# Kernel tuning notes

Hardware: AMD Instinct MI355X
Metric: run time of the kernel (lower is better)

Reference implementation:

```python
import jax, jax.numpy as jnp
import numpy as np

FILTER_SIZE = 7
IMG = 256
MID = FILTER_SIZE // 2
# base coefficient per tap: -((r-m)^2 + (c-m)^2) / 2, flattened over the k*k window
_BASE = np.array([-(((r - MID) ** 2 + (c - MID) ** 2) / 2.0)
                  for r in range(FILTER_SIZE) for c in range(FILTER_SIZE)],
                 dtype=np.float32)


def setup_inputs() -> dict:
    key = jax.random.key(0)
    k1, k2 = jax.random.split(key)
    x = jax.random.normal(k1, (16, 3, IMG, IMG), dtype=jnp.float32)
    sigma = jax.random.uniform(k2, (16, 3, IMG, IMG), dtype=jnp.float32)
    return {"x": x, "sigma": sigma}


def reference(x, sigma):
    base = jnp.asarray(_BASE)  # (k2,)
    # exp(base * sigma^2) normalized over the k2 taps == softmax over tap axis
    logits = base[:, None, None, None, None] * (sigma * sigma)[None]  # (k2,B,3,H,W)
    w = jax.nn.softmax(logits, axis=0)  # (k2,B,3,H,W)
    xp = jnp.pad(x, ((0, 0), (0, 0), (MID, MID), (MID, MID)), mode="reflect")
    result = jnp.zeros_like(x)
    i = 0
    for r in range(FILTER_SIZE):
        for c in range(FILTER_SIZE):
            result = result + xp[:, :, r:r + IMG, c:c + IMG] * w[i]
            i += 1
    return result
```

## Files before the change

### kernel.cpp

```cpp
#include <hip/hip_runtime.h>

#define IMG 256
#define TX 64
#define TY 16
#define LH 22
#define LSTRIDE 72
#define NCHUNK (LH * (LSTRIDE / 4))

__device__ __forceinline__ int reflect_idx(int i) {
    i = i < 0 ? -i : i;
    i = i > (IMG - 1) ? 2 * (IMG - 1) - i : i;
    return i;
}

__global__ __launch_bounds__(256)
void agf_kernel(const float* __restrict__ x, const float* __restrict__ sigma,
                float* __restrict__ out) {
    __shared__ float tile[LH * LSTRIDE];

    const int plane = blockIdx.z;
    const int gx0 = blockIdx.x * TX;
    const int gy0 = blockIdx.y * TY;
    const int tid = threadIdx.x;

    const float* xp = x + (size_t)plane * (IMG * IMG);

    #pragma unroll
    for (int it = 0; it < 2; ++it) {
        const int idx = tid + it * 256;
        if (idx < NCHUNK) {
            const int lr = idx / 18;
            const int lc4 = idx - lr * 18;
            const int lcol = lc4 * 4;
            const int grow = reflect_idx(gy0 - 3 + lr);
            const int gcol = gx0 - 4 + lcol;
            const float* src = xp + (size_t)grow * IMG;
            if (gcol >= 0 && gcol <= IMG - 4) {
                *reinterpret_cast<float4*>(&tile[lr * LSTRIDE + lcol]) =
                    *reinterpret_cast<const float4*>(src + gcol);
            } else {
                #pragma unroll
                for (int j = 0; j < 4; ++j)
                    tile[lr * LSTRIDE + lcol + j] = src[reflect_idx(gcol + j)];
            }
        }
    }
    __syncthreads();

    const int tx = tid & 15;
    const int ty = tid >> 4;
    const int col0 = tx * 4;
    const int gy = gy0 + ty;
    const size_t gbase = (size_t)plane * (IMG * IMG) + (size_t)gy * IMG + gx0 + col0;

    const float4 sg = *reinterpret_cast<const float4*>(sigma + gbase);
    const float s[4] = {sg.x, sg.y, sg.z, sg.w};

    float e1[4], e2[4], e3[4], inv[4], acc[4];
    #pragma unroll
    for (int p = 0; p < 4; ++p) {
        const float s2 = s[p] * s[p];
        const float a = __expf(-0.5f * s2);
        const float t = a * a;
        const float b = t * t;
        const float c = b * b * a;
        e1[p] = a; e2[p] = b; e3[p] = c;
        const float S = 1.0f + 2.0f * (a + b + c);
        inv[p] = __builtin_amdgcn_rcpf(S * S);
        acc[p] = 0.0f;
    }

    auto rsum = [&](const float v[12], int p) {
        return v[p + 4]
             + e1[p] * (v[p + 3] + v[p + 5])
             + e2[p] * (v[p + 2] + v[p + 6])
             + e3[p] * (v[p + 1] + v[p + 7]);
    };

    #pragma unroll
    for (int q = 0; q < 3; ++q) {
        const float* rowA = &tile[(ty + q) * LSTRIDE + col0];
        const float* rowB = &tile[(ty + 6 - q) * LSTRIDE + col0];
        const float4 a0 = *reinterpret_cast<const float4*>(rowA);
        const float4 a1 = *reinterpret_cast<const float4*>(rowA + 4);
        const float4 a2 = *reinterpret_cast<const float4*>(rowA + 8);
        const float4 b0 = *reinterpret_cast<const float4*>(rowB);
        const float4 b1 = *reinterpret_cast<const float4*>(rowB + 4);
        const float4 b2 = *reinterpret_cast<const float4*>(rowB + 8);
        const float vs[12] = {a0.x + b0.x, a0.y + b0.y, a0.z + b0.z, a0.w + b0.w,
                              a1.x + b1.x, a1.y + b1.y, a1.z + b1.z, a1.w + b1.w,
                              a2.x + b2.x, a2.y + b2.y, a2.z + b2.z, a2.w + b2.w};
        #pragma unroll
        for (int p = 0; p < 4; ++p) {
            const float er = (q == 0) ? e3[p] : (q == 1) ? e2[p] : e1[p];
            acc[p] += er * rsum(vs, p);
        }
    }
    {
        const float* rowC = &tile[(ty + 3) * LSTRIDE + col0];
        const float4 c0 = *reinterpret_cast<const float4*>(rowC);
        const float4 c1 = *reinterpret_cast<const float4*>(rowC + 4);
        const float4 c2 = *reinterpret_cast<const float4*>(rowC + 8);
        const float vc[12] = {c0.x, c0.y, c0.z, c0.w,
                              c1.x, c1.y, c1.z, c1.w,
                              c2.x, c2.y, c2.z, c2.w};
        #pragma unroll
        for (int p = 0; p < 4; ++p)
            acc[p] += rsum(vc, p);
    }

    float4 o;
    o.x = acc[0] * inv[0];
    o.y = acc[1] * inv[1];
    o.z = acc[2] * inv[2];
    o.w = acc[3] * inv[3];
    *reinterpret_cast<float4*>(out + gbase) = o;
}

extern "C" void kernel_launch(void* const* d_in, const int* in_sizes, int n_in,
                              void* d_out, int out_size, void* d_ws, size_t ws_size,
                              hipStream_t stream) {
    const float* x = (const float*)d_in[0];
    const float* sigma = (const float*)d_in[1];
    float* out = (float*)d_out;

    const int planes = in_sizes[0] / (IMG * IMG);
    dim3 grid(IMG / TX, IMG / TY, planes);
    agf_kernel<<<grid, 256, 0, stream>>>(x, sigma, out);
}
```

Before: 85.16 us.

## Compute two output rows per thread with shared LDS row loads across them

```diff
diff --git a/kernel.cpp b/kernel.cpp
--- a/kernel.cpp
+++ b/kernel.cpp
@@ -2,8 +2,8 @@
 
 #define IMG 256
 #define TX 64
-#define TY 16
-#define LH 22
+#define TY 32
+#define LH 38
 #define LSTRIDE 72
 #define NCHUNK (LH * (LSTRIDE / 4))
 
@@ -11,6 +11,29 @@
     i = i < 0 ? -i : i;
     i = i > (IMG - 1) ? 2 * (IMG - 1) - i : i;
     return i;
+}
+
+__device__ __forceinline__ void loadrow(const float* __restrict__ rp, float d[12]) {
+    const float4 q0 = *reinterpret_cast<const float4*>(rp);
+    const float4 q1 = *reinterpret_cast<const float4*>(rp + 4);
+    const float4 q2 = *reinterpret_cast<const float4*>(rp + 8);
+    d[0] = q0.x; d[1] = q0.y; d[2]  = q0.z; d[3]  = q0.w;
+    d[4] = q1.x; d[5] = q1.y; d[6]  = q1.z; d[7]  = q1.w;
+    d[8] = q2.x; d[9] = q2.y; d[10] = q2.z; d[11] = q2.w;
+}
+
+__device__ __forceinline__ void fold(const float u[12], const float v[12], float d[12]) {
+    #pragma unroll
+    for (int j = 0; j < 12; ++j) d[j] = u[j] + v[j];
+}
+
+__device__ __forceinline__ float rsum(const float v[12], int p,
+                                      const float e1[4], const float e2[4],
+                                      const float e3[4]) {
+    return v[p + 4]
+         + e1[p] * (v[p + 3] + v[p + 5])
+         + e2[p] * (v[p + 2] + v[p + 6])
+         + e3[p] * (v[p + 1] + v[p + 7]);
 }
 
 __global__ __launch_bounds__(256)
@@ -26,7 +49,7 @@
     const float* xp = x + (size_t)plane * (IMG * IMG);
 
     #pragma unroll
-    for (int it = 0; it < 2; ++it) {
+    for (int it = 0; it < 3; ++it) {
         const int idx = tid + it * 256;
         if (idx < NCHUNK) {
             const int lr = idx / 18;
@@ -48,73 +71,92 @@
     __syncthreads();
 
     const int tx = tid & 15;
-    const int ty = tid >> 4;
+    const int ty = (tid >> 4) * 2;
     const int col0 = tx * 4;
     const int gy = gy0 + ty;
     const size_t gbase = (size_t)plane * (IMG * IMG) + (size_t)gy * IMG + gx0 + col0;
 
-    const float4 sg = *reinterpret_cast<const float4*>(sigma + gbase);
-    const float s[4] = {sg.x, sg.y, sg.z, sg.w};
+    const float4 sg0 = *reinterpret_cast<const float4*>(sigma + gbase);
+    const float4 sg1 = *reinterpret_cast<const float4*>(sigma + gbase + IMG);
+    const float s0v[4] = {sg0.x, sg0.y, sg0.z, sg0.w};
+    const float s1v[4] = {sg1.x, sg1.y, sg1.z, sg1.w};
 
-    float e1[4], e2[4], e3[4], inv[4], acc[4];
+    float e1a[4], e2a[4], e3a[4], inva[4];
+    float e1b[4], e2b[4], e3b[4], invb[4];
     #pragma unroll
     for (int p = 0; p < 4; ++p) {
-        const float s2 = s[p] * s[p];
-        const float a = __expf(-0.5f * s2);
-        const float t = a * a;
-        const float b = t * t;
-        const float c = b * b * a;
-        e1[p] = a; e2[p] = b; e3[p] = c;
-        const float S = 1.0f + 2.0f * (a + b + c);
-        inv[p] = __builtin_amdgcn_rcpf(S * S);
-        acc[p] = 0.0f;
+        {
+            const float s2 = s0v[p] * s0v[p];
+            const float a = __expf(-0.5f * s2);
+            const float t = a * a;
+            const float b = t * t;
+            const float c = b * b * a;
+            e1a[p] = a; e2a[p] = b; e3a[p] = c;
+            const float S = 1.0f + 2.0f * (a + b + c);
+            inva[p] = __builtin_amdgcn_rcpf(S * S);
+        }
+        {
+            const float s2 = s1v[p] * s1v[p];
+            const float a = __expf(-0.5f * s2);
+            const float t = a * a;
+            const float b = t * t;
+            const float c = b * b * a;
+            e1b[p] = a; e2b[p] = b; e3b[p] = c;
+            const float S = 1.0f + 2.0f * (a + b + c);
+            invb[p] = __builtin_amdgcn_rcpf(S * S);
+        }
     }
 
-    auto rsum = [&](const float v[12], int p) {
-        return v[p + 4]
-             + e1[p] * (v[p + 3] + v[p + 5])
-             + e2[p] * (v[p + 2] + v[p + 6])
-             + e3[p] * (v[p + 1] + v[p + 7]);
-    };
+    const float* tbase = &tile[ty * LSTRIDE + col0];
+
+    float acc0[4] = {0.f, 0.f, 0.f, 0.f};
+    float acc1[4] = {0.f, 0.f, 0.f, 0.f};
+    float ra[12], rb[12], rc[12], rf[12];
+
+    loadrow(tbase + 1 * LSTRIDE, ra);
+    loadrow(tbase + 7 * LSTRIDE, rb);
+    fold(ra, rb, rf);
+    #pragma unroll
+    for (int p = 0; p < 4; ++p) acc1[p] += e3b[p] * rsum(rf, p, e1b, e2b, e3b);
+
+    loadrow(tbase + 5 * LSTRIDE, rb);
+    fold(ra, rb, rf);
+    #pragma unroll
+    for (int p = 0; p < 4; ++p) acc0[p] += e2a[p] * rsum(rf, p, e1a, e2a, e3a);
+
+    loadrow(tbase + 3 * LSTRIDE, ra);
+    fold(ra, rb, rf);
+    #pragma unroll
+    for (int p = 0; p < 4; ++p) acc1[p] += e1b[p] * rsum(rf, p, e1b, e2b, e3b);
+
+    loadrow(tbase + 0 * LSTRIDE, rb);
+    loadrow(tbase + 6 * LSTRIDE, rc);
+    fold(rb, rc, rf);
+    #pragma unroll
+    for (int p = 0; p < 4; ++p) acc0[p] += e3a[p] * rsum(rf, p, e1a, e2a, e3a);
+
+    loadrow(tbase + 2 * LSTRIDE, rb);
+    fold(rb, rc, rf);
+    #pragma unroll
+    for (int p = 0; p < 4; ++p) acc1[p] += e2b[p] * rsum(rf, p, e1b, e2b, e3b);
+
+    loadrow(tbase + 4 * LSTRIDE, rc);
+    fold(rb, rc, rf);
+    #pragma unroll
+    for (int p = 0; p < 4; ++p) acc0[p] += e1a[p] * rsum(rf, p, e1a, e2a, e3a);
 
     #pragma unroll
-    for (int q = 0; q < 3; ++q) {
-        const float* rowA = &tile[(ty + q) * LSTRIDE + col0];
-        const float* rowB = &tile[(ty + 6 - q) * LSTRIDE + col0];
-        const float4 a0 = *reinterpret_cast<const float4*>(rowA);
-        const float4 a1 = *reinterpret_cast<const float4*>(rowA + 4);
-        const float4 a2 = *reinterpret_cast<const float4*>(rowA + 8);
-        const float4 b0 = *reinterpret_cast<const float4*>(rowB);
-        const float4 b1 = *reinterpret_cast<const float4*>(rowB + 4);
-        const float4 b2 = *reinterpret_cast<const float4*>(rowB + 8);
-        const float vs[12] = {a0.x + b0.x, a0.y + b0.y, a0.z + b0.z, a0.w + b0.w,
-                              a1.x + b1.x, a1.y + b1.y, a1.z + b1.z, a1.w + b1.w,
-                              a2.x + b2.x, a2.y + b2.y, a2.z + b2.z, a2.w + b2.w};
-        #pragma unroll
-        for (int p = 0; p < 4; ++p) {
-            const float er = (q == 0) ? e3[p] : (q == 1) ? e2[p] : e1[p];
-            acc[p] += er * rsum(vs, p);
-        }
-    }
-    {
-        const float* rowC = &tile[(ty + 3) * LSTRIDE + col0];
-        const float4 c0 = *reinterpret_cast<const float4*>(rowC);
-        const float4 c1 = *reinterpret_cast<const float4*>(rowC + 4);
-        const float4 c2 = *reinterpret_cast<const float4*>(rowC + 8);
-        const float vc[12] = {c0.x, c0.y, c0.z, c0.w,
-                              c1.x, c1.y, c1.z, c1.w,
-                              c2.x, c2.y, c2.z, c2.w};
-        #pragma unroll
-        for (int p = 0; p < 4; ++p)
-            acc[p] += rsum(vc, p);
-    }
+    for (int p = 0; p < 4; ++p) acc0[p] += rsum(ra, p, e1a, e2a, e3a);
+    #pragma unroll
+    for (int p = 0; p < 4; ++p) acc1[p] += rsum(rc, p, e1b, e2b, e3b);
 
-    float4 o;
-    o.x = acc[0] * inv[0];
-    o.y = acc[1] * inv[1];
-    o.z = acc[2] * inv[2];
-    o.w = acc[3] * inv[3];
-    *reinterpret_cast<float4*>(out + gbase) = o;
+    float4 o0, o1;
+    o0.x = acc0[0] * inva[0]; o0.y = acc0[1] * inva[1];
+    o0.z = acc0[2] * inva[2]; o0.w = acc0[3] * inva[3];
+    o1.x = acc1[0] * invb[0]; o1.y = acc1[1] * invb[1];
+    o1.z = acc1[2] * invb[2]; o1.w = acc1[3] * invb[3];
+    *reinterpret_cast<float4*>(out + gbase) = o0;
+    *reinterpret_cast<float4*>(out + gbase + IMG) = o1;
 }
 
 extern "C" void kernel_launch(void* const* d_in, const int* in_sizes, int n_in,
```

New measurement: 81.50 us. 1.04x faster.
